# Performance work log

Hardware: AMD Instinct MI355X
Metric: run time of the kernel (lower is better)

Reference implementation:

```python
import jax, jax.numpy as jnp
import numpy as np

B, T, I = 256, 512, 12   # batch, n_step, input_dims
H, Z = 1024, 128         # hidden_dims, z1_dims


def _gru_step(h, xt, Wih, Whh, bih, bhh):
    # torch GRU/GRUCell gate math; gate order in weights: r, z, n
    gi = xt @ Wih.T + bih            # [B, 3H]
    gh = h @ Whh.T + bhh             # [B, 3H]
    i_r, i_z, i_n = jnp.split(gi, 3, axis=-1)
    h_r, h_z, h_n = jnp.split(gh, 3, axis=-1)
    r = jax.nn.sigmoid(i_r + h_r)
    zg = jax.nn.sigmoid(i_z + h_z)
    n = jnp.tanh(i_n + r * h_n)
    return (1.0 - zg) * n + zg * h


def setup_inputs() -> dict:
    key = jax.random.key(0)
    ks = jax.random.split(key, 24)
    s = 0.03
    d = {
        "x": jax.random.uniform(ks[0], (B, T, I), dtype=jnp.float32),
        "noise": jax.random.normal(ks[1], (B, Z), dtype=jnp.float32),
        # bidirectional GRU encoder (forward / backward directions)
        "W_ih_f": jax.random.normal(ks[2], (3 * H, I)) * s,
        "W_hh_f": jax.random.normal(ks[3], (3 * H, H)) * s,
        "b_ih_f": jnp.zeros((3 * H,), jnp.float32),
        "b_hh_f": jnp.zeros((3 * H,), jnp.float32),
        "W_ih_b": jax.random.normal(ks[4], (3 * H, I)) * s,
        "W_hh_b": jax.random.normal(ks[5], (3 * H, H)) * s,
        "b_ih_b": jnp.zeros((3 * H,), jnp.float32),
        "b_hh_b": jnp.zeros((3 * H,), jnp.float32),
        # mu / var heads over concatenated bidirectional final state [B, 2H]
        "W_mu": jax.random.normal(ks[6], (Z, 2 * H)) * s,
        "b_mu": jnp.zeros((Z,), jnp.float32),
        "W_var": jax.random.normal(ks[7], (Z, 2 * H)) * s,
        "b_var": jnp.zeros((Z,), jnp.float32),
        # decoder
        "W_init": jax.random.normal(ks[8], (H, Z)) * s,
        "b_init": jnp.zeros((H,), jnp.float32),
        "W_out": jax.random.normal(ks[9], (I, H)) * s,
        "b_out": jnp.zeros((I,), jnp.float32),
        "Wc_ih": jax.random.normal(ks[10], (3 * H, I + Z)) * s,
        "Wc_hh": jax.random.normal(ks[11], (3 * H, H)) * s,
        "bc_ih": jnp.zeros((3 * H,), jnp.float32),
        "bc_hh": jnp.zeros((3 * H,), jnp.float32),
    }
    return d


def reference(x, noise, W_ih_f, W_hh_f, b_ih_f, b_hh_f,
              W_ih_b, W_hh_b, b_ih_b, b_hh_b,
              W_mu, b_mu, W_var, b_var,
              W_init, b_init, W_out, b_out,
              Wc_ih, Wc_hh, bc_ih, bc_hh):
    b, t, i = x.shape
    h0 = jnp.zeros((b, W_hh_f.shape[1]), x.dtype)
    xs = jnp.swapaxes(x, 0, 1)  # [T, B, I]

    # ---- encoder: bidirectional GRU, keep only final hidden per direction ----
    def step_f(h, xt):
        return _gru_step(h, xt, W_ih_f, W_hh_f, b_ih_f, b_hh_f), None

    def step_b(h, xt):
        return _gru_step(h, xt, W_ih_b, W_hh_b, b_ih_b, b_hh_b), None

    h_f, _ = jax.lax.scan(step_f, h0, xs)
    h_b, _ = jax.lax.scan(step_b, h0, xs[::-1])
    henc = jnp.concatenate([h_f, h_b], axis=-1)  # [B, 2H] (dir-major, matches torch view)

    mean = henc @ W_mu.T + b_mu
    stddev = jnp.exp(0.5 * (henc @ W_var.T + b_var))
    z = mean + stddev * noise  # rsample (training mode)

    # ---- decoder: GRUCell with teacher forcing (eps starts at 1 -> p < eps) ----
    init_out = jnp.zeros((b, i), x.dtype).at[:, -1].set(1.0)
    teacher = jnp.concatenate([init_out[:, None, :], x[:, :-1, :]], axis=1)  # [B,T,I]
    inps = jnp.swapaxes(teacher, 0, 1)  # [T, B, I]

    hx = jnp.tanh(z @ W_init.T + b_init)

    def dstep(h, inp):
        u = jnp.concatenate([inp, z], axis=1)  # [B, I+Z]
        h = _gru_step(h, u, Wc_ih, Wc_hh, bc_ih, bc_hh)
        out = jax.nn.sigmoid(h @ W_out.T + b_out)
        return h, out

    _, outs = jax.lax.scan(dstep, hx, inps)  # outs: [T, B, I]
    recon = jnp.swapaxes(outs, 0, 1)  # [B, T, I]
    return recon, mean, stddev
```

## Files before the change

### kernel.cpp

```cpp
#include <hip/hip_runtime.h>
#include <cstdint>
#include <cstddef>


typedef _Float16 f16;
typedef _Float16 f16x8 __attribute__((ext_vector_type(8)));
typedef float f32x4 __attribute__((ext_vector_type(4)));

#define NB 256
#define NT 512
#define NI 12
#define NH 1024
#define NZ 128
#define NG 3072
#define KE_ENC 1056
#define KE_DEC 1184
#define XK_ENC 32
#define XK_DEC 160
#define ZXP 40

#define MFMA16(a, b, c) __builtin_amdgcn_mfma_f32_16x16x32_f16((a), (b), (c), 0, 0, 0)

#define OFF_WMF   ((size_t)0)
#define OFF_WMB   (OFF_WMF + (size_t)NG * KE_ENC * 2)
#define OFF_WMD   (OFF_WMB + (size_t)NG * KE_ENC * 2)
#define OFF_WNF   (OFF_WMD + (size_t)NG * KE_DEC * 2)
#define OFF_WNB   (OFF_WNF + (size_t)NH * XK_ENC * 2)
#define OFF_WND   (OFF_WNB + (size_t)NH * XK_ENC * 2)
#define OFF_WOUT  (OFF_WND + (size_t)NH * XK_DEC * 2)
#define OFF_HENC16 (OFF_WOUT + (size_t)16 * KE_ENC * 2)
#define OFF_HF32   (OFF_HENC16 + (size_t)4 * NB * NH * 2)
#define OFF_CTL    (OFF_HF32 + (size_t)2 * NB * NH * 4)
#define OFF_H32D   (OFF_CTL + (size_t)2 * NB * NH * 2)
#define OFF_Z32    (OFF_H32D + (size_t)NB * NH * 4)
#define OFF_Z16    (OFF_Z32 + (size_t)NB * NZ * 4)
#define OFF_FLG    (OFF_Z16 + (size_t)NB * NZ * 2)
#define N_FLG 204800
#define N_FLGD 131072
#define WS_NEEDED (OFF_FLG + (size_t)N_FLG * 4)

#define OUT_MEAN (NB * NT * NI)
#define OUT_STD  (OUT_MEAN + NB * NZ)

__device__ __forceinline__ void wave_spin(const unsigned* base, unsigned tgt,
                                          int lane, int nslots) {
    const unsigned* p = base + (lane & (nslots - 1));
    for (;;) {
        unsigned v = __hip_atomic_load(p, __ATOMIC_RELAXED, __HIP_MEMORY_SCOPE_AGENT);
        if (__all((int)(v == tgt))) break;
        __builtin_amdgcn_s_sleep(1);
    }
}

#define PW(N) do { \
    asm volatile("s_waitcnt vmcnt(%0)" :: "n"(N) : "memory"); \
    __builtin_amdgcn_sched_barrier(0x387); \
} while (0)

__global__ __launch_bounds__(256) void prep_kernel(
    const float* __restrict__ Whhf, const float* __restrict__ Wihf,
    const float* __restrict__ bihf, const float* __restrict__ bhhf,
    const float* __restrict__ Whhb, const float* __restrict__ Wihb,
    const float* __restrict__ bihb, const float* __restrict__ bhhb,
    const float* __restrict__ Wchh, const float* __restrict__ Wcih,
    const float* __restrict__ bcih, const float* __restrict__ bchh,
    const float* __restrict__ Wo,   const float* __restrict__ bo,
    f16* __restrict__ wmf, f16* __restrict__ wmb, f16* __restrict__ wmd,
    f16* __restrict__ wnf, f16* __restrict__ wnb, f16* __restrict__ wnd,
    f16* __restrict__ wout,
    f16* __restrict__ h16e0f, f16* __restrict__ h16e0b,
    unsigned* __restrict__ flgs, unsigned* __restrict__ flgd)
{
    const int gsz = gridDim.x * blockDim.x;
    const int gid = blockIdx.x * blockDim.x + threadIdx.x;

    for (int idx = gid; idx < NG * KE_ENC; idx += gsz) {
        const int c = idx / KE_ENC, k = idx - c * KE_ENC;
        float vf, vb;
        if (k < NH) { vf = Whhf[c * NH + k]; vb = Whhb[c * NH + k]; }
        else {
            const int e = k - NH;
            if (c < 2 * NH) {
                if (e < 12)       { vf = Wihf[c * 12 + e]; vb = Wihb[c * 12 + e]; }
                else if (e == 12) { vf = bihf[c] + bhhf[c]; vb = bihb[c] + bhhb[c]; }
                else              { vf = 0.f; vb = 0.f; }
            } else {
                vf = (e == 12) ? bhhf[c] : 0.f;
                vb = (e == 12) ? bhhb[c] : 0.f;
            }
        }
        wmf[idx] = (f16)vf; wmb[idx] = (f16)vb;
    }
    for (int idx = gid; idx < NG * KE_DEC; idx += gsz) {
        const int c = idx / KE_DEC, k = idx - c * KE_DEC;
        float v;
        if (k < NH) v = Wchh[c * NH + k];
        else {
            const int e = k - NH;
            if (c < 2 * NH) {
                if (e < 12)       v = Wcih[c * 140 + e];
                else if (e == 12) v = bcih[c] + bchh[c];
                else if (e < 32)  v = 0.f;
                else              v = Wcih[c * 140 + 12 + (e - 32)];
            } else v = (e == 12) ? bchh[c] : 0.f;
        }
        wmd[idx] = (f16)v;
    }
    for (int idx = gid; idx < NH * XK_ENC; idx += gsz) {
        const int j = idx >> 5, e = idx & 31;
        const int c = 2 * NH + j;
        float vf, vb;
        if (e < 12)       { vf = Wihf[c * 12 + e]; vb = Wihb[c * 12 + e]; }
        else if (e == 12) { vf = bihf[c]; vb = bihb[c]; }
        else              { vf = 0.f; vb = 0.f; }
        wnf[idx] = (f16)vf; wnb[idx] = (f16)vb;
    }
    for (int idx = gid; idx < NH * XK_DEC; idx += gsz) {
        const int j = idx / XK_DEC, e = idx - j * XK_DEC;
        const int c = 2 * NH + j;
        float v;
        if (e < 12)       v = Wcih[c * 140 + e];
        else if (e == 12) v = bcih[c];
        else if (e < 32)  v = 0.f;
        else              v = Wcih[c * 140 + 12 + (e - 32)];
        wnd[idx] = (f16)v;
    }
    for (int idx = gid; idx < 16 * KE_ENC; idx += gsz) {
        const int i = idx / KE_ENC, k = idx - i * KE_ENC;
        float v = 0.f;
        if (i < 12) {
            if (k < NH) v = Wo[i * NH + k];
            else if (k == NH + 12) v = bo[i];
        }
        wout[idx] = (f16)v;
    }
    for (int idx = gid; idx < NB * NH; idx += gsz) {
        h16e0f[idx] = (f16)0.f; h16e0b[idx] = (f16)0.f;
    }
    for (int idx = gid; idx < N_FLG; idx += gsz) flgs[idx] = 0u;
    for (int idx = gid; idx < N_FLGD; idx += gsz) flgd[idx] = 0u;
}

template<int MODE>
__global__ __launch_bounds__(256, 1) void persist_kernel(
    const float* __restrict__ x,
    const f16* __restrict__ wmF, const f16* __restrict__ wmB_,
    const f16* __restrict__ wnF, const f16* __restrict__ wnB_,
    const f16* __restrict__ wout, const f16* __restrict__ z16,
    f16* __restrict__ hbuf,
    float* __restrict__ hf32,
    const float* __restrict__ h32i,
    float* __restrict__ dout,
    unsigned* __restrict__ flg)
{
    constexpr int KE  = MODE ? KE_DEC : KE_ENC;
    constexpr int KEP = KE + 8;
    constexpr int XK  = MODE ? XK_DEC : XK_ENC;
    constexpr int XKP = XK + 8;
    constexpr int NZT = MODE ? 4 : 0;
    constexpr int NRT = MODE ? 1 : 2;
    constexpr int MROWS = MODE ? 64 : 128;

    __shared__ f16 Wlds[48 * KEP];
    __shared__ f16 Zx[MROWS * ZXP];
    __shared__ f16 wnlds[16 * XKP];
    __shared__ f16 wolds[MODE ? 16 * 1064 : 8];

    const int tid = threadIdx.x;
    const int bid = blockIdx.x;
    const int w = tid >> 6, lane = tid & 63;
    const int lr = lane & 15, quad = lane >> 4;

    const int chain = bid >> 6;
    const int slice = bid & 63;
    const int dir = MODE ? 0 : (chain >> 1);
    const int m0 = MODE ? chain * 64 : (chain & 1) * 128;
    const int j0 = slice * 16;
    const bool outw = (MODE == 1) && (slice == 0);
    const int RB = m0 + (MODE ? (w << 4) : (w << 5));

    const f16* wm = (MODE == 0 && dir) ? wmB_ : wmF;
    const f16* wn = (MODE == 0 && dir) ? wnB_ : wnF;
    f16* hb0 = hbuf + (MODE ? (size_t)0 : (size_t)dir * 2 * NB * NH);
    constexpr int BMSK = MODE ? 3 : 1;

    constexpr int KQ = KE / 8;
    for (int u = tid; u < 48 * KQ; u += 256) {
        const int r = u / KQ, kk = u - r * KQ;
        const int c = (r >> 4) * NH + j0 + (r & 15);
        *(uint4*)&Wlds[r * KEP + kk * 8] = *(const uint4*)(wm + (size_t)c * KE + kk * 8);
    }
    constexpr int XQ = XK / 8;
    for (int u = tid; u < 16 * XQ; u += 256) {
        const int r = u / XQ, kk = u - r * XQ;
        *(uint4*)&wnlds[r * XKP + kk * 8] =
            *(const uint4*)(wn + (size_t)(j0 + r) * XK + kk * 8);
    }
    if (outw) {
        for (int u = tid; u < 16 * 132; u += 256) {
            const int r = u / 132, kk = u - r * 132;
            *(uint4*)&wolds[r * 1064 + kk * 8] =
                *(const uint4*)(wout + (size_t)r * KE_ENC + kk * 8);
        }
    }
    for (int u = tid; u < MROWS * ZXP / 8; u += 256)
        *(uint4*)&Zx[u * 8] = make_uint4(0u, 0u, 0u, 0u);
    __syncthreads();

    float hmast[2][4];
    f16x8 azr[2][NZT ? NZT : 1];
#pragma unroll
    for (int rt = 0; rt < NRT; ++rt)
#pragma unroll
        for (int r = 0; r < 4; ++r)
            hmast[rt][r] = MODE
                ? h32i[(size_t)(RB + rt * 16 + quad * 4 + r) * NH + j0 + lr]
                : 0.f;
    if (MODE) {
#pragma unroll
        for (int rt = 0; rt < NRT; ++rt)
#pragma unroll
            for (int zt = 0; zt < NZT; ++zt)
                azr[rt][zt] = *(const f16x8*)(z16 +
                    (size_t)(RB + rt * 16 + lr) * NZ + zt * 32 + (quad << 3));
    }
    f16x8 ax;
#pragma unroll
    for (int j = 0; j < 8; ++j) ax[j] = (f16)0.f;
    if (quad == 1) ax[4] = (f16)1.f;

    unsigned* myflg = flg + (size_t)chain * 512 * 64;

#define AISSUE_E(c) do { \
    asm volatile( \
        "global_load_dwordx4 %0, %4, off offset:%6 sc0 sc1\n\t" \
        "global_load_dwordx4 %1, %5, off offset:%6 sc0 sc1\n\t" \
        "global_load_dwordx4 %2, %4, off offset:%7 sc0 sc1\n\t" \
        "global_load_dwordx4 %3, %5, off offset:%7 sc0 sc1" \
        : "=&v"(av[(c) & 15][0]), "=&v"(av[(c) & 15][1]), \
          "=&v"(av[(c) & 15][2]), "=&v"(av[(c) & 15][3]) \
        : "v"(ga0), "v"(ga1), "n"((c) * 128), "n"((c) * 128 + 64) \
        : "memory"); \
} while (0)
#define PCONS_E(c) do { \
    _Pragma("unroll") \
    for (int kt2_ = 0; kt2_ < 2; ++kt2_) { \
        const f16x8 a0_ = av[(c) & 15][kt2_ * 2]; \
        const f16x8 a1_ = av[(c) & 15][kt2_ * 2 + 1]; \
        _Pragma("unroll") \
        for (int g_ = 0; g_ < 3; ++g_) { \
            const f16x8 b_ = *(const f16x8*)(&Wlds[(g_ * 16 + lr) * KEP + ((c) * 2 + kt2_) * 32 + (quad << 3)]); \
            acc[g_][0] = MFMA16(a0_, b_, acc[g_][0]); \
            acc[g_][1] = MFMA16(a1_, b_, acc[g_][1]); \
        } \
    } \
} while (0)
#define AISSUE_D(c) do { \
    asm volatile( \
        "global_load_dwordx4 %0, %2, off offset:%3 sc0 sc1\n\t" \
        "global_load_dwordx4 %1, %2, off offset:%4 sc0 sc1" \
        : "=&v"(av[(c)][0]), "=&v"(av[(c)][1]) \
        : "v"(ga0), "n"((c) * 128), "n"((c) * 128 + 64) \
        : "memory"); \
} while (0)
#define PCONS_D(c) do { \
    _Pragma("unroll") \
    for (int kt2_ = 0; kt2_ < 2; ++kt2_) { \
        const f16x8 a0_ = av[(c)][kt2_]; \
        _Pragma("unroll") \
        for (int g_ = 0; g_ < 3; ++g_) { \
            const f16x8 b_ = *(const f16x8*)(&Wlds[(g_ * 16 + lr) * KEP + ((c) * 2 + kt2_) * 32 + (quad << 3)]); \
            acc[g_][0] = MFMA16(a0_, b_, acc[g_][0]); \
        } \
        if (outw) { \
            const f16x8 bo_ = *(const f16x8*)(&wolds[lr * 1064 + ((c) * 2 + kt2_) * 32 + (quad << 3)]); \
            accq = MFMA16(a0_, bo_, accq); \
        } \
    } \
} while (0)
#define OCONSQ(c) do { \
    _Pragma("unroll") \
    for (int kt2_ = 0; kt2_ < 2; ++kt2_) { \
        const f16x8 bo_ = *(const f16x8*)(&wolds[lr * 1064 + ((c) * 2 + kt2_) * 32 + (quad << 3)]); \
        accq = MFMA16(av[(c)][kt2_], bo_, accq); \
    } \
} while (0)

#pragma unroll 1
    for (int t = 0; t < NT; ++t) {
        if (tid < MROWS) {
            f16 rowv[16];
            if (MODE == 1 && t == 0) {
#pragma unroll
                for (int e = 0; e < 12; ++e) rowv[e] = (f16)((e == NI - 1) ? 1.f : 0.f);
            } else {
                const int b_ = m0 + tid;
                const int tx = MODE ? (t - 1) : (dir ? (NT - 1 - t) : t);
                const float4* xr = (const float4*)(x + ((size_t)b_ * NT + tx) * NI);
                const float4 x0 = xr[0], x1 = xr[1], x2 = xr[2];
                rowv[0] = (f16)x0.x; rowv[1] = (f16)x0.y; rowv[2] = (f16)x0.z; rowv[3] = (f16)x0.w;
                rowv[4] = (f16)x1.x; rowv[5] = (f16)x1.y; rowv[6] = (f16)x1.z; rowv[7] = (f16)x1.w;
                rowv[8] = (f16)x2.x; rowv[9] = (f16)x2.y; rowv[10] = (f16)x2.z; rowv[11] = (f16)x2.w;
            }
            rowv[12] = (f16)1.f; rowv[13] = (f16)0.f; rowv[14] = (f16)0.f; rowv[15] = (f16)0.f;
            *(uint4*)&Zx[tid * ZXP]     = *(const uint4*)&rowv[0];
            *(uint4*)&Zx[tid * ZXP + 8] = *(const uint4*)&rowv[8];
        }
        if (t > 0 && tid < 64)
            wave_spin(myflg + (size_t)(t - 1) * 64, (unsigned)t, lane, 64);
        __syncthreads();

        const f16* hcur = hb0 + (size_t)(t & BMSK) * (NB * NH);
        const char* ga0 = (const char*)(hcur +
            (size_t)(RB + lr) * NH) + (quad << 4);
        const char* ga1 = ga0 + (size_t)16 * NH * 2;
        (void)ga1;

        f32x4 acc[3][2], accn[2];
#pragma unroll
        for (int g = 0; g < 3; ++g)
#pragma unroll
            for (int rt = 0; rt < 2; ++rt) { f32x4 zv = {0.f,0.f,0.f,0.f}; acc[g][rt] = zv; }
        { f32x4 zv = {0.f,0.f,0.f,0.f}; accn[0] = zv; accn[1] = zv; }
        f32x4 accq = {0.f, 0.f, 0.f, 0.f};

        if (MODE == 0) {
            f16x8 av[16][4];
            AISSUE_E(0);  AISSUE_E(1);  AISSUE_E(2);  AISSUE_E(3);
            AISSUE_E(4);  AISSUE_E(5);  AISSUE_E(6);  AISSUE_E(7);
            AISSUE_E(8);  AISSUE_E(9);
            PW(36); PCONS_E(0);  AISSUE_E(10);
            PW(36); PCONS_E(1);  AISSUE_E(11);
            PW(36); PCONS_E(2);  AISSUE_E(12);
            PW(36); PCONS_E(3);  AISSUE_E(13);
            PW(36); PCONS_E(4);  AISSUE_E(14);
            PW(36); PCONS_E(5);  AISSUE_E(15);
            PW(36); PCONS_E(6);
            PW(32); PCONS_E(7);
            PW(28); PCONS_E(8);
            PW(24); PCONS_E(9);
            PW(20); PCONS_E(10);
            PW(16); PCONS_E(11);
            PW(12); PCONS_E(12);
            PW(8);  PCONS_E(13);
            PW(4);  PCONS_E(14);
            PW(0);  PCONS_E(15);
        } else {
            f16x8 av[16][2];
            AISSUE_D(0);  AISSUE_D(1);  AISSUE_D(2);  AISSUE_D(3);
            AISSUE_D(4);  AISSUE_D(5);  AISSUE_D(6);  AISSUE_D(7);
            AISSUE_D(8);  AISSUE_D(9);  AISSUE_D(10); AISSUE_D(11);
            AISSUE_D(12); AISSUE_D(13); AISSUE_D(14); AISSUE_D(15);
            PW(30); PCONS_D(0);
            PW(28); PCONS_D(1);
            PW(26); PCONS_D(2);
            PW(24); PCONS_D(3);
            PW(22); PCONS_D(4);
            PW(20); PCONS_D(5);
            PW(18); PCONS_D(6);
            PW(16); PCONS_D(7);
            PW(14); PCONS_D(8);
            PW(12); PCONS_D(9);
            PW(10); PCONS_D(10);
            PW(8);  PCONS_D(11);
            PW(6);  PCONS_D(12);
            PW(4);  PCONS_D(13);
            PW(2);  PCONS_D(14);
            PW(0);  PCONS_D(15);
        }

#pragma unroll
        for (int xt = 0; xt <= NZT; ++xt) {
            const int kt = 32 + xt;
            f16x8 a0, a1;
            if (xt == 0) {
                a0 = *(const f16x8*)(&Zx[((MODE ? (w << 4) : (w << 5)) + lr) * ZXP + (quad << 3)]);
                if (MODE == 0)
                    a1 = *(const f16x8*)(&Zx[((w << 5) + 16 + lr) * ZXP + (quad << 3)]);
            } else { a0 = azr[0][xt - 1]; if (NRT > 1) a1 = azr[1][xt - 1]; }
#pragma unroll
            for (int g = 0; g < 3; ++g) {
                f16x8 b = *(const f16x8*)(&Wlds[(g * 16 + lr) * KEP + kt * 32 + (quad << 3)]);
                acc[g][0] = MFMA16(a0, b, acc[g][0]);
                if (NRT > 1) acc[g][1] = MFMA16(a1, b, acc[g][1]);
            }
            f16x8 bn = *(const f16x8*)(&wnlds[lr * XKP + xt * 32 + (quad << 3)]);
            accn[0] = MFMA16(a0, bn, accn[0]);
            if (NRT > 1) accn[1] = MFMA16(a1, bn, accn[1]);
        }

        if (outw) {
            const f16x8 bo_ = *(const f16x8*)(&wolds[lr * 1064 + 1024 + (quad << 3)]);
            accq = MFMA16(ax, bo_, accq);
            if (t >= 1 && lr < NI) {
#pragma unroll
                for (int r = 0; r < 4; ++r) {
                    const int b_ = RB + quad * 4 + r;
                    dout[(size_t)b_ * (NT * NI) + (t - 1) * NI + lr] =
                        1.f / (1.f + __expf(-accq[r]));
                }
            }
        }

        f16* hnext = hb0 + (size_t)((t + 1) & BMSK) * (NB * NH);
#pragma unroll
        for (int rt = 0; rt < NRT; ++rt) {
#pragma unroll
            for (int r = 0; r < 4; ++r) {
                const float rr  = acc[0][rt][r];
                const float zz  = acc[1][rt][r];
                const float ghn = acc[2][rt][r];
                const float gin = accn[rt][r];
                const float rg = 1.f / (1.f + __expf(-rr));
                const float zg = 1.f / (1.f + __expf(-zz));
                const float nv = gin + rg * ghn;
                const float e2 = __expf(2.f * nv);
                const float th = 1.f - 2.f / (e2 + 1.f);
                const float hn = (1.f - zg) * th + zg * hmast[rt][r];
                hmast[rt][r] = hn;
                const unsigned hv =
                    (unsigned)__builtin_bit_cast(unsigned short, (f16)hn);
                const unsigned ov = (unsigned)__shfl_xor((int)hv, 1, 64);
                if (!(lr & 1)) {
                    const int row = RB + rt * 16 + quad * 4 + r;
                    __hip_atomic_store(
                        (unsigned*)&hnext[(size_t)row * NH + j0 + lr],
                        hv | (ov << 16),
                        __ATOMIC_RELAXED, __HIP_MEMORY_SCOPE_AGENT);
                }
            }
        }
        __syncthreads();
        if (tid == 0)
            __hip_atomic_store(myflg + (size_t)t * 64 + slice, (unsigned)(t + 1),
                               __ATOMIC_RELAXED, __HIP_MEMORY_SCOPE_AGENT);
    }

    if (MODE == 0) {
        float* hdst = hf32 + (size_t)dir * NB * NH;
#pragma unroll
        for (int rt = 0; rt < NRT; ++rt)
#pragma unroll
            for (int r = 0; r < 4; ++r) {
                const int row = RB + rt * 16 + quad * 4 + r;
                hdst[(size_t)row * NH + j0 + lr] = hmast[rt][r];
            }
    }

    if (MODE == 1 && outw) {
        if (tid < 64)
            wave_spin(myflg + (size_t)511 * 64, 512u, lane, 64);
        __syncthreads();
        const f16* hc = hb0 + (size_t)(512 & BMSK) * (NB * NH);
        const char* ga0 = (const char*)(hc + (size_t)(RB + lr) * NH) + (quad << 4);
        f32x4 accq = {0.f, 0.f, 0.f, 0.f};
        f16x8 av[16][2];
        AISSUE_D(0);  AISSUE_D(1);  AISSUE_D(2);  AISSUE_D(3);
        AISSUE_D(4);  AISSUE_D(5);  AISSUE_D(6);  AISSUE_D(7);
        AISSUE_D(8);  AISSUE_D(9);  AISSUE_D(10); AISSUE_D(11);
        AISSUE_D(12); AISSUE_D(13); AISSUE_D(14); AISSUE_D(15);
        PW(30); OCONSQ(0);
        PW(28); OCONSQ(1);
        PW(26); OCONSQ(2);
        PW(24); OCONSQ(3);
        PW(22); OCONSQ(4);
        PW(20); OCONSQ(5);
        PW(18); OCONSQ(6);
        PW(16); OCONSQ(7);
        PW(14); OCONSQ(8);
        PW(12); OCONSQ(9);
        PW(10); OCONSQ(10);
        PW(8);  OCONSQ(11);
        PW(6);  OCONSQ(12);
        PW(4);  OCONSQ(13);
        PW(2);  OCONSQ(14);
        PW(0);  OCONSQ(15);
        {
            const f16x8 bo_ = *(const f16x8*)(&wolds[lr * 1064 + 1024 + (quad << 3)]);
            accq = MFMA16(ax, bo_, accq);
        }
        if (lr < NI) {
#pragma unroll
            for (int r = 0; r < 4; ++r) {
                const int b_ = RB + quad * 4 + r;
                dout[(size_t)b_ * (NT * NI) + 511 * NI + lr] =
                    1.f / (1.f + __expf(-accq[r]));
            }
        }
    }
#undef AISSUE_E
#undef PCONS_E
#undef AISSUE_D
#undef PCONS_D
#undef OCONSQ
}

__global__ __launch_bounds__(256) void heads1_kernel(
    const float* __restrict__ hf, const float* __restrict__ hb,
    const float* __restrict__ Wmu, const float* __restrict__ bmu,
    const float* __restrict__ Wvar, const float* __restrict__ bvar,
    const float* __restrict__ noise,
    float* __restrict__ dout, float* __restrict__ z32, f16* __restrict__ z16)
{
    const int tid = threadIdx.x;
    const int b  = ((int)blockIdx.x >> 3) * 16 + (tid >> 4);
    const int zi = ((int)blockIdx.x & 7) * 16 + (tid & 15);
    const float4* h4 = (const float4*)(hf + (size_t)b * NH);
    const float4* g4 = (const float4*)(hb + (size_t)b * NH);
    const float4* m4 = (const float4*)(Wmu + (size_t)zi * (2 * NH));
    const float4* v4 = (const float4*)(Wvar + (size_t)zi * (2 * NH));
    float sm_ = 0.f, sv = 0.f;
    for (int k = 0; k < NH / 4; ++k) {
        const float4 h = h4[k], a = m4[k], c = v4[k];
        sm_ += h.x * a.x + h.y * a.y + h.z * a.z + h.w * a.w;
        sv  += h.x * c.x + h.y * c.y + h.z * c.z + h.w * c.w;
    }
    for (int k = 0; k < NH / 4; ++k) {
        const float4 h = g4[k], a = m4[NH / 4 + k], c = v4[NH / 4 + k];
        sm_ += h.x * a.x + h.y * a.y + h.z * a.z + h.w * a.w;
        sv  += h.x * c.x + h.y * c.y + h.z * c.z + h.w * c.w;
    }
    const float mean = sm_ + bmu[zi];
    const float lv   = sv + bvar[zi];
    const float sd   = __expf(0.5f * lv);
    const float zv   = mean + sd * noise[(size_t)b * NZ + zi];
    dout[OUT_MEAN + (size_t)b * NZ + zi] = mean;
    dout[OUT_STD  + (size_t)b * NZ + zi] = sd;
    z32[b * NZ + zi] = zv;
    z16[b * NZ + zi] = (f16)zv;
}

__global__ __launch_bounds__(256) void heads2_kernel(
    const float* __restrict__ z32, const float* __restrict__ Winit,
    const float* __restrict__ binit,
    float* __restrict__ h32d, f16* __restrict__ h16d)
{
    __shared__ float Wi[16 * NZ];
    __shared__ float bi[16];
    const int tid = threadIdx.x;
    const int jb = blockIdx.x;
    for (int f = tid; f < 16 * NZ; f += 256)
        Wi[f] = Winit[(size_t)(jb * 16 + (f >> 7)) * NZ + (f & 127)];
    if (tid < 16) bi[tid] = binit[jb * 16 + tid];
    __syncthreads();
    const int b = tid;
    const float4* z4 = (const float4*)(z32 + (size_t)b * NZ);
    float4 zr[NZ / 4];
#pragma unroll
    for (int k = 0; k < NZ / 4; ++k) zr[k] = z4[k];
    for (int hj = 0; hj < 16; ++hj) {
        const float4* w4 = (const float4*)(Wi + hj * NZ);
        float s = bi[hj];
#pragma unroll
        for (int k = 0; k < NZ / 4; ++k) {
            const float4 a = w4[k], z = zr[k];
            s += z.x * a.x + z.y * a.y + z.z * a.z + z.w * a.w;
        }
        const float e2 = __expf(2.f * s);
        const float th = 1.f - 2.f / (e2 + 1.f);
        h32d[(size_t)b * NH + jb * 16 + hj] = th;
        h16d[(size_t)b * NH + jb * 16 + hj] = (f16)th;
    }
}

extern "C" void kernel_launch(void* const* d_in, const int* in_sizes, int n_in,
                              void* d_out, int out_size, void* d_ws, size_t ws_size,
                              hipStream_t stream)
{
    const float* x     = (const float*)d_in[0];
    const float* noise = (const float*)d_in[1];
    const float* Wihf  = (const float*)d_in[2];
    const float* Whhf  = (const float*)d_in[3];
    const float* bihf  = (const float*)d_in[4];
    const float* bhhf  = (const float*)d_in[5];
    const float* Wihb  = (const float*)d_in[6];
    const float* Whhb  = (const float*)d_in[7];
    const float* bihb  = (const float*)d_in[8];
    const float* bhhb  = (const float*)d_in[9];
    const float* Wmu   = (const float*)d_in[10];
    const float* bmu   = (const float*)d_in[11];
    const float* Wvar  = (const float*)d_in[12];
    const float* bvar  = (const float*)d_in[13];
    const float* Winit = (const float*)d_in[14];
    const float* binit = (const float*)d_in[15];
    const float* Wo    = (const float*)d_in[16];
    const float* bo    = (const float*)d_in[17];
    const float* Wcih  = (const float*)d_in[18];
    const float* Wchh  = (const float*)d_in[19];
    const float* bcih  = (const float*)d_in[20];
    const float* bchh  = (const float*)d_in[21];
    float* dout = (float*)d_out;
    char*  ws   = (char*)d_ws;

    if (ws_size < WS_NEEDED) return;

    f16* wmf  = (f16*)(ws + OFF_WMF);
    f16* wmb  = (f16*)(ws + OFF_WMB);
    f16* wmd  = (f16*)(ws + OFF_WMD);
    f16* wnf  = (f16*)(ws + OFF_WNF);
    f16* wnb  = (f16*)(ws + OFF_WNB);
    f16* wnd  = (f16*)(ws + OFF_WND);
    f16* wo16 = (f16*)(ws + OFF_WOUT);
    f16* h16  = (f16*)(ws + OFF_HENC16);
    float* hf32  = (float*)(ws + OFF_HF32);
    float* h32d  = (float*)(ws + OFF_H32D);
    float* z32p  = (float*)(ws + OFF_Z32);
    f16*   z16p  = (f16*)(ws + OFF_Z16);
    unsigned* flg_e = (unsigned*)(ws + OFF_FLG);
    unsigned* flg_d = (unsigned*)(ws + OFF_CTL);

    prep_kernel<<<2048, 256, 0, stream>>>(
        Whhf, Wihf, bihf, bhhf, Whhb, Wihb, bihb, bhhb,
        Wchh, Wcih, bcih, bchh, Wo, bo,
        wmf, wmb, wmd, wnf, wnb, wnd, wo16,
        h16 , h16 + (size_t)2 * NB * NH ,
        flg_e, flg_d);

    persist_kernel<0><<<256, 256, 0, stream>>>(
        x, wmf, wmb, wnf, wnb, (const f16*)nullptr, (const f16*)nullptr,
        h16, hf32, (const float*)nullptr, dout, flg_e);

    heads1_kernel<<<128, 256, 0, stream>>>(hf32, hf32 + (size_t)NB * NH,
                                           Wmu, bmu, Wvar, bvar, noise,
                                           dout, z32p, z16p);
    heads2_kernel<<<64, 256, 0, stream>>>(z32p, Winit, binit, h32d, h16 );

    persist_kernel<1><<<256, 256, 0, stream>>>(
        x, wmd, (const f16*)nullptr, wnd, (const f16*)nullptr, wo16, z16p,
        h16, (float*)nullptr, h32d, dout, flg_d);
}
```

Baseline: 9.095 ms.

## Add dedicated encoder kernel with half weights in LDS and half streamed

Replaces the templated persistent kernel for the encoder with a specialized enc_kernel. Each block keeps 48 rows of the recurrent weights resident in LDS and streams the other 16-column slice from global memory in a software-pipelined schedule of inline-asm loads interleaved with MFMA. The hidden-state loads bypass caches via sc0/sc1, and input projection uses a small padded Zx tile. This aims to widen the per-block output slice to 32 columns while coping with the LDS capacity limit, at the cost of extra global weight traffic each step and fragile hand-scheduled waits.

```diff
diff --git a/kernel.cpp b/kernel.cpp
--- a/kernel.cpp
+++ b/kernel.cpp
@@ -139,6 +139,220 @@
     }
     for (int idx = gid; idx < N_FLG; idx += gsz) flgs[idx] = 0u;
     for (int idx = gid; idx < N_FLGD; idx += gsz) flgd[idx] = 0u;
+}
+
+__global__ __launch_bounds__(256, 1) void enc_kernel(
+    const float* __restrict__ x,
+    const f16* __restrict__ wmF, const f16* __restrict__ wmB_,
+    const f16* __restrict__ wnF, const f16* __restrict__ wnB_,
+    f16* __restrict__ hbuf,
+    float* __restrict__ hf32,
+    unsigned* __restrict__ flg)
+{
+    constexpr int KE  = KE_ENC;
+    constexpr int KEP = KE + 8;
+
+    __shared__ f16 Wlds[48 * KEP];
+    __shared__ f16 wext[48 * 36];
+    __shared__ f16 wnlds[32 * ZXP];
+    __shared__ f16 Zx[64 * ZXP];
+
+    const int tid = threadIdx.x;
+    const int bid = blockIdx.x;
+    const int w = tid >> 6, lane = tid & 63;
+    const int lr = lane & 15, quad = lane >> 4;
+
+    const int chain = bid >> 5;
+    const int slice = bid & 31;
+    const int dir = chain >> 2;
+    const int m0 = (chain & 3) * 64;
+    const int j0 = slice * 32;
+    const int RB = m0 + (w << 4);
+
+    const f16* wm = dir ? wmB_ : wmF;
+    const f16* wn = dir ? wnB_ : wnF;
+    f16* hb0 = hbuf + (size_t)dir * 2 * NB * NH;
+
+    constexpr int KQ = KE / 8;
+    for (int u = tid; u < 48 * KQ; u += 256) {
+        const int r = u / KQ, kk = u - r * KQ;
+        const int c = (r >> 4) * NH + j0 + (r & 15);
+        *(uint4*)&Wlds[r * KEP + kk * 8] = *(const uint4*)(wm + (size_t)c * KE + kk * 8);
+    }
+    for (int u = tid; u < 48 * 4; u += 256) {
+        const int r = u >> 2, kk = u & 3;
+        const int c = (r >> 4) * NH + j0 + 16 + (r & 15);
+        *(uint4*)&wext[r * 36 + kk * 8] = *(const uint4*)(wm + (size_t)c * KE + 1024 + kk * 8);
+    }
+    for (int u = tid; u < 32 * 4; u += 256) {
+        const int r = u >> 2, kk = u & 3;
+        *(uint4*)&wnlds[r * ZXP + kk * 8] = *(const uint4*)(wn + (size_t)(j0 + r) * XK_ENC + kk * 8);
+    }
+    for (int u = tid; u < 64 * ZXP / 8; u += 256)
+        *(uint4*)&Zx[u * 8] = make_uint4(0u, 0u, 0u, 0u);
+    __syncthreads();
+
+    float hmast[2][4];
+#pragma unroll
+    for (int cs = 0; cs < 2; ++cs)
+#pragma unroll
+        for (int r = 0; r < 4; ++r) hmast[cs][r] = 0.f;
+
+    unsigned* myflg = flg + (size_t)chain * 512 * 32;
+
+    const char* bg0 = (const char*)wm + 2 * ((size_t)(0 * NH + j0 + 16 + lr) * KE + (quad << 3));
+    const char* bg1 = (const char*)wm + 2 * ((size_t)(1 * NH + j0 + 16 + lr) * KE + (quad << 3));
+    const char* bg2 = (const char*)wm + 2 * ((size_t)(2 * NH + j0 + 16 + lr) * KE + (quad << 3));
+
+#define EA(c) do { \
+    asm volatile( \
+        "global_load_dwordx4 %0, %2, off offset:%3 sc0 sc1\n\t" \
+        "global_load_dwordx4 %1, %2, off offset:%4 sc0 sc1" \
+        : "=&v"(av[(c) & 7][0]), "=&v"(av[(c) & 7][1]) \
+        : "v"(ga0), "n"((c) * 128), "n"((c) * 128 + 64) \
+        : "memory"); \
+} while (0)
+#define EB(c) do { \
+    asm volatile( \
+        "global_load_dwordx4 %0, %6, off offset:%9\n\t" \
+        "global_load_dwordx4 %1, %6, off offset:%10\n\t" \
+        "global_load_dwordx4 %2, %7, off offset:%9\n\t" \
+        "global_load_dwordx4 %3, %7, off offset:%10\n\t" \
+        "global_load_dwordx4 %4, %8, off offset:%9\n\t" \
+        "global_load_dwordx4 %5, %8, off offset:%10" \
+        : "=&v"(bv[(c) & 3][0]), "=&v"(bv[(c) & 3][1]), \
+          "=&v"(bv[(c) & 3][2]), "=&v"(bv[(c) & 3][3]), \
+          "=&v"(bv[(c) & 3][4]), "=&v"(bv[(c) & 3][5]) \
+        : "v"(bg0), "v"(bg1), "v"(bg2), "n"((c) * 128), "n"((c) * 128 + 64) \
+        : "memory"); \
+} while (0)
+#define ECONS(c) do { \
+    _Pragma("unroll") \
+    for (int kt2_ = 0; kt2_ < 2; ++kt2_) { \
+        const int ktg_ = (c) * 2 + kt2_; \
+        const f16x8 a_ = av[(c) & 7][kt2_]; \
+        _Pragma("unroll") \
+        for (int g_ = 0; g_ < 3; ++g_) { \
+            const f16x8 bl_ = *(const f16x8*)(&Wlds[(g_ * 16 + lr) * KEP + ktg_ * 32 + (quad << 3)]); \
+            acc0[g_] = MFMA16(a_, bl_, acc0[g_]); \
+            acc1[g_] = MFMA16(a_, bv[(c) & 3][g_ * 2 + kt2_], acc1[g_]); \
+        } \
+    } \
+} while (0)
+
+#pragma unroll 1
+    for (int t = 0; t < NT; ++t) {
+        if (tid < 64) {
+            f16 rowv[16];
+            const int b_ = m0 + tid;
+            const int tx = dir ? (NT - 1 - t) : t;
+            const float4* xr = (const float4*)(x + ((size_t)b_ * NT + tx) * NI);
+            const float4 x0 = xr[0], x1 = xr[1], x2 = xr[2];
+            rowv[0] = (f16)x0.x; rowv[1] = (f16)x0.y; rowv[2] = (f16)x0.z; rowv[3] = (f16)x0.w;
+            rowv[4] = (f16)x1.x; rowv[5] = (f16)x1.y; rowv[6] = (f16)x1.z; rowv[7] = (f16)x1.w;
+            rowv[8] = (f16)x2.x; rowv[9] = (f16)x2.y; rowv[10] = (f16)x2.z; rowv[11] = (f16)x2.w;
+            rowv[12] = (f16)1.f; rowv[13] = (f16)0.f; rowv[14] = (f16)0.f; rowv[15] = (f16)0.f;
+            *(uint4*)&Zx[tid * ZXP]     = *(const uint4*)&rowv[0];
+            *(uint4*)&Zx[tid * ZXP + 8] = *(const uint4*)&rowv[8];
+        }
+        if (t > 0 && tid < 64)
+            wave_spin(myflg + (size_t)(t - 1) * 32, (unsigned)t, lane, 32);
+        __syncthreads();
+
+        const f16* hcur = hb0 + (size_t)(t & 1) * (NB * NH);
+        const char* ga0 = (const char*)(hcur + (size_t)(RB + lr) * NH) + (quad << 4);
+
+        f32x4 acc0[3], acc1[3];
+#pragma unroll
+        for (int g = 0; g < 3; ++g) {
+            f32x4 zv = {0.f, 0.f, 0.f, 0.f};
+            acc0[g] = zv; acc1[g] = zv;
+        }
+        f32x4 accn0 = {0.f, 0.f, 0.f, 0.f}, accn1 = {0.f, 0.f, 0.f, 0.f};
+
+        f16x8 av[8][2];
+        f16x8 bv[4][6];
+        EA(0); EA(1); EA(2); EA(3); EA(4);
+        EB(0); EB(1); EB(2);
+        PW(12); EA(5);  EB(3);  ECONS(0);
+        PW(14); EA(6);  EB(4);  ECONS(1);
+        PW(16); EA(7);  EB(5);  ECONS(2);
+        PW(16); EA(8);  EB(6);  ECONS(3);
+        PW(16); EA(9);  EB(7);  ECONS(4);
+        PW(16); EA(10); EB(8);  ECONS(5);
+        PW(16); EA(11); EB(9);  ECONS(6);
+        PW(16); EA(12); EB(10); ECONS(7);
+        PW(16); EA(13); EB(11); ECONS(8);
+        PW(16); EA(14); EB(12); ECONS(9);
+        PW(16); EA(15); EB(13); ECONS(10);
+        PW(16); EB(14); ECONS(11);
+        PW(14); EB(15); ECONS(12);
+        PW(12); ECONS(13);
+        PW(6);  ECONS(14);
+        PW(0);  ECONS(15);
+
+        {
+            const f16x8 a0 = *(const f16x8*)(&Zx[((w << 4) + lr) * ZXP + (quad << 3)]);
+#pragma unroll
+            for (int g = 0; g < 3; ++g) {
+                const f16x8 bl = *(const f16x8*)(&Wlds[(g * 16 + lr) * KEP + 1024 + (quad << 3)]);
+                acc0[g] = MFMA16(a0, bl, acc0[g]);
+                const f16x8 bs = *(const f16x8*)(&wext[(g * 16 + lr) * 36 + (quad << 3)]);
+                acc1[g] = MFMA16(a0, bs, acc1[g]);
+            }
+            const f16x8 bn0 = *(const f16x8*)(&wnlds[lr * ZXP + (quad << 3)]);
+            accn0 = MFMA16(a0, bn0, accn0);
+            const f16x8 bn1 = *(const f16x8*)(&wnlds[(16 + lr) * ZXP + (quad << 3)]);
+            accn1 = MFMA16(a0, bn1, accn1);
+        }
+
+        f16* hnext = hb0 + (size_t)((t + 1) & 1) * (NB * NH);
+#pragma unroll
+        for (int cs = 0; cs < 2; ++cs) {
+#pragma unroll
+            for (int r = 0; r < 4; ++r) {
+                const float rr  = cs ? acc1[0][r] : acc0[0][r];
+                const float zz  = cs ? acc1[1][r] : acc0[1][r];
+                const float ghn = cs ? acc1[2][r] : acc0[2][r];
+                const float gin = cs ? accn1[r]   : accn0[r];
+                const float rg = 1.f / (1.f + __expf(-rr));
+                const float zg = 1.f / (1.f + __expf(-zz));
+                const float nv = gin + rg * ghn;
+                const float e2 = __expf(2.f * nv);
+                const float th = 1.f - 2.f / (e2 + 1.f);
+                const float hn = (1.f - zg) * th + zg * hmast[cs][r];
+                hmast[cs][r] = hn;
+                const unsigned hv =
+                    (unsigned)__builtin_bit_cast(unsigned short, (f16)hn);
+                const unsigned ov = (unsigned)__shfl_xor((int)hv, 1, 64);
+                if (!(lr & 1)) {
+                    const int row = RB + quad * 4 + r;
+                    __hip_atomic_store(
+                        (unsigned*)&hnext[(size_t)row * NH + j0 + cs * 16 + lr],
+                        hv | (ov << 16),
+                        __ATOMIC_RELAXED, __HIP_MEMORY_SCOPE_AGENT);
+                }
+            }
+        }
+        __syncthreads();
+        if (tid == 0)
+            __hip_atomic_store(myflg + (size_t)t * 32 + slice, (unsigned)(t + 1),
+                               __ATOMIC_RELAXED, __HIP_MEMORY_SCOPE_AGENT);
+    }
+#undef EA
+#undef EB
+#undef ECONS
+
+    {
+        float* hdst = hf32 + (size_t)dir * NB * NH;
+#pragma unroll
+        for (int cs = 0; cs < 2; ++cs)
+#pragma unroll
+            for (int r = 0; r < 4; ++r) {
+                const int row = RB + quad * 4 + r;
+                hdst[(size_t)row * NH + j0 + cs * 16 + lr] = hmast[cs][r];
+            }
+    }
 }
 
 template<int MODE>
@@ -616,9 +830,8 @@
         h16 , h16 + (size_t)2 * NB * NH ,
         flg_e, flg_d);
 
-    persist_kernel<0><<<256, 256, 0, stream>>>(
-        x, wmf, wmb, wnf, wnb, (const f16*)nullptr, (const f16*)nullptr,
-        h16, hf32, (const float*)nullptr, dout, flg_e);
+    enc_kernel<<<256, 256, 0, stream>>>(
+        x, wmf, wmb, wnf, wnb, h16, hf32, flg_e);
 
     heads1_kernel<<<128, 256, 0, stream>>>(hf32, hf32 + (size_t)NB * NH,
                                            Wmu, bmu, Wvar, bvar, noise,
```

New measurement: 9.902 ms. 1.09x slower.
